# Kernel tuning notes

Hardware: AMD Instinct MI355X
Metric: run time of the kernel (lower is better)

Reference implementation:

```python
import jax, jax.numpy as jnp
import numpy as np

VOCAB, EMBED, HIDDEN, OUT = 50257, 256, 256, 2
BATCH, SEQ = 128, 512


def setup_inputs() -> dict:
    key = jax.random.key(0)
    ks = jax.random.split(key, 8)
    tokens = jax.random.randint(ks[0], (BATCH, SEQ), 0, VOCAB)
    emb = jax.random.normal(ks[1], (VOCAB, EMBED), jnp.float32) * 0.02
    emb = emb.at[VOCAB - 1].set(0.0)  # padding_idx=-1 -> last row zeroed
    s_x = 1.0 / np.sqrt(EMBED)
    s_h = 1.0 / np.sqrt(HIDDEN)
    # gates stacked in order (f, i, c, o): W_x=[W_f;W_i;W_c;W_o], same for U/biases
    W_x = jax.random.uniform(ks[2], (4 * HIDDEN, EMBED), jnp.float32, -s_x, s_x)
    U_h = jax.random.uniform(ks[3], (4 * HIDDEN, HIDDEN), jnp.float32, -s_h, s_h)
    b_x = jax.random.uniform(ks[4], (4 * HIDDEN,), jnp.float32, -s_x, s_x)
    b_u = jax.random.uniform(ks[5], (4 * HIDDEN,), jnp.float32, -s_h, s_h)
    b_g = jnp.zeros((4 * HIDDEN,), jnp.float32)  # extra b_f/b_i/b_c/b_o params
    fc_w = jax.random.uniform(ks[6], (OUT, HIDDEN), jnp.float32, -s_h, s_h)
    fc_b = jax.random.uniform(ks[7], (OUT,), jnp.float32, -s_h, s_h)
    return {"tokens": tokens, "emb": emb, "W_x": W_x, "b_x": b_x,
            "U_h": U_h, "b_u": b_u, "b_g": b_g, "fc_w": fc_w, "fc_b": fc_b}


def reference(tokens, emb, W_x, b_x, U_h, b_u, b_g, fc_w, fc_b):
    H = U_h.shape[1]
    x = emb[tokens]                                   # [B,S,E]
    # precompute all input projections + all constant biases in one GEMM
    xp = jnp.einsum('bse,ge->bsg', x, W_x) + (b_x + b_u + b_g)  # [B,S,4H]
    xp = jnp.swapaxes(xp, 0, 1)                       # [S,B,4H]
    B = tokens.shape[0]
    h0 = jnp.zeros((B, H), x.dtype)
    c0 = jnp.zeros((B, H), x.dtype)

    def step(carry, xp_t):
        h, c = carry
        g = xp_t + h @ U_h.T                          # [B,4H]
        f = jax.nn.sigmoid(g[:, 0 * H:1 * H])
        i = jax.nn.sigmoid(g[:, 1 * H:2 * H])
        c_hat = jnp.tanh(g[:, 2 * H:3 * H])
        o = jax.nn.sigmoid(g[:, 3 * H:4 * H])
        c = f * c + i * c_hat
        h = o * jnp.tanh(c)
        return (h, c), None

    (h_t, _), _ = jax.lax.scan(step, (h0, c0), xp)
    return h_t @ fc_w.T + fc_b                        # [B,OUT]
```

## Files before the change

kernel.cpp:

```cpp
#include <hip/hip_runtime.h>

typedef short short8 __attribute__((ext_vector_type(8)));
typedef float f4 __attribute__((ext_vector_type(4)));

#define BATCH 128
#define SEQ   512
#define EMB   256
#define HID   256
#define G4    1024

static __device__ __forceinline__ unsigned short f2b(float f) {
    union { float f; unsigned int u; } v; v.f = f;
    unsigned int u = v.u;
    return (unsigned short)((u + 0x7FFFu + ((u >> 16) & 1u)) >> 16);
}
static __device__ __forceinline__ float b2f(unsigned short s) {
    union { unsigned int u; float f; } v; v.u = ((unsigned int)s) << 16;
    return v.f;
}

__global__ void prep_kernel(const float* __restrict__ W_x, const float* __restrict__ U_h,
                            const float* __restrict__ b_x, const float* __restrict__ b_u,
                            const float* __restrict__ b_g,
                            unsigned short* __restrict__ w_xb, unsigned short* __restrict__ u_hb,
                            float* __restrict__ bias,
                            unsigned int* __restrict__ hx32, float* __restrict__ out) {
    int i = blockIdx.x * blockDim.x + threadIdx.x;
    if (i < G4 * EMB) w_xb[i] = f2b(W_x[i]);
    if (i < G4 * HID) u_hb[i] = f2b(U_h[i]);
    if (i < G4) bias[i] = b_x[i] + b_u[i] + b_g[i];
    if (i < 65536) hx32[i] = 0;
    if (i < 256) out[i] = 0.0f;
}

__global__ __launch_bounds__(256) void xp_gemm(
    const int* __restrict__ tokens, const float* __restrict__ emb,
    const unsigned short* __restrict__ w_xb, const float* __restrict__ bias,
    unsigned short* __restrict__ xp)
{
    __shared__ unsigned short As[64][264];
    __shared__ unsigned short Bs[64][264];
    __shared__ unsigned short Xs[64][72];
    const int m0 = blockIdx.x * 64;
    const int b  = m0 >> 9;
    const int s0 = m0 & 511;
    const int tid = threadIdx.x;
    const int cS = tid >> 2, qS = (tid & 3) * 64;
    {
        const int tok = tokens[m0 + cS];
        const float* src = emb + (long)tok * EMB + qS;
        #pragma unroll
        for (int i = 0; i < 8; ++i) {
            float4 v0 = ((const float4*)src)[2 * i];
            float4 v1 = ((const float4*)src)[2 * i + 1];
            short8 pk;
            pk[0] = (short)f2b(v0.x); pk[1] = (short)f2b(v0.y);
            pk[2] = (short)f2b(v0.z); pk[3] = (short)f2b(v0.w);
            pk[4] = (short)f2b(v1.x); pk[5] = (short)f2b(v1.y);
            pk[6] = (short)f2b(v1.z); pk[7] = (short)f2b(v1.w);
            *(short8*)&As[cS][qS + i * 8] = pk;
        }
    }
    __syncthreads();
    const int w = tid >> 6, l = tid & 63;
    const int ln = l & 15, hi = l >> 4;
    short8 a[8];
    #pragma unroll
    for (int kk = 0; kk < 8; ++kk)
        a[kk] = *(const short8*)&As[16 * w + ln][kk * 32 + hi * 8];

    const int rl = tid >> 2;
    const int cl = (tid & 3) * 16;

    for (int n0 = 0; n0 < G4; n0 += 64) {
        {
            const unsigned short* src = &w_xb[(size_t)(n0 + cS) * EMB + qS];
            #pragma unroll
            for (int i = 0; i < 8; ++i)
                *(short8*)&Bs[cS][qS + i * 8] = *(const short8*)&src[i * 8];
        }
        __syncthreads();
        f4 acc[4] = {};
        #pragma unroll
        for (int kk = 0; kk < 8; ++kk) {
            #pragma unroll
            for (int nn = 0; nn < 4; ++nn) {
                short8 bfr = *(const short8*)&Bs[nn * 16 + ln][kk * 32 + hi * 8];
                acc[nn] = __builtin_amdgcn_mfma_f32_16x16x32_bf16(a[kk], bfr, acc[nn], 0, 0, 0);
            }
        }
        #pragma unroll
        for (int nn = 0; nn < 4; ++nn) {
            const float bs = bias[n0 + nn * 16 + ln];
            #pragma unroll
            for (int r = 0; r < 4; ++r)
                Xs[16 * w + 4 * hi + r][nn * 16 + ln] = f2b(acc[nn][r] + bs);
        }
        size_t off = ((size_t)(s0 + rl) * BATCH + b) * G4 + n0 + cl;
        *(short8*)&xp[off]     = *(const short8*)&Xs[rl][cl];
        *(short8*)&xp[off + 8] = *(const short8*)&Xs[rl][cl + 8];
        __syncthreads();
    }
}

__global__ void __launch_bounds__(512, 2)
lstm_recur(const unsigned short* __restrict__ xp,
           const unsigned short* __restrict__ u_hb,
           const float* __restrict__ fc_w, const float* __restrict__ fc_b,
           unsigned int* __restrict__ hxw, float* __restrict__ out)
{
    __shared__ unsigned short hsl0[4096];
    __shared__ unsigned short hsl1[4096];
    __shared__ unsigned short xl0[16 * 136];
    __shared__ unsigned short xl1[16 * 136];
    const int tid = threadIdx.x;
    const int w = tid >> 6, l = tid & 63;
    const int ln = l & 15, hi = l >> 4;
    const int bid = blockIdx.x;
    const int g = bid & 7, E = bid >> 3;
    const int lu = w * 4 + hi;

    short8 Br[8];
    int fo[8];
    {
        const int col = (ln & 3) * 256 + E * 32 + w * 4 + (ln >> 2);
        const unsigned short* ubase = u_hb + (size_t)col * HID + hi * 8;
        #pragma unroll
        for (int j = 0; j < 8; ++j) {
            const int s = (E + j) & 7;
            fo[j] = s * 512;
            Br[j] = *(const short8*)&ubase[s * 32];
        }
    }

    for (int i = tid; i < 2048; i += 512) { ((unsigned*)hsl0)[i] = 0; ((unsigned*)hsl1)[i] = 0; }

    const int xrow = tid >> 5, seg4 = tid & 31;
    const size_t xoff = (size_t)(16 * g + xrow) * 1024 + (seg4 >> 3) * 256 + E * 32 + (seg4 & 7) * 4;
    const int xdst = xrow * 136 + (seg4 >> 3) * 32 + (seg4 & 7) * 4;
    *(unsigned long long*)&xl0[xdst] = *(const unsigned long long*)(xp + xoff);
    __syncthreads();

    int pbase[2], pub[2];
    #pragma unroll
    for (int par = 0; par < 2; ++par) {
        pbase[par] = ((par * 8 + g) * 8) * 512 + tid;
        pub[par]   = ((par * 8 + g) * 8 + E) * 512 + lu * 16 + ln;
    }
    int ppq[7];
    #pragma unroll
    for (int d = 0; d < 7; ++d) ppq[d] = (((E + 1 + d) & 7) << 9);
    const int lup = tid >> 4, bp = tid & 15;
    const int sbase = ((lup >> 3) * 16 + bp) * 8 + (lup & 7);
    const int ho = E * 512 + ((lu >> 3) * 16 + ln) * 8 + (lu & 7);
    const int xb = ln * 136 + lu;
    const int fro = l * 8;

    float c0 = 0.0f;

    for (int t = 0; t < SEQ; ++t) {
        const int cur = t & 1;
        unsigned short* hslc = cur ? hsl1 : hsl0;
        unsigned short* hsln = cur ? hsl0 : hsl1;
        const unsigned short* xlc = cur ? xl1 : xl0;
        unsigned short* xln = cur ? xl0 : xl1;

        unsigned int pw[7];
        const unsigned int* ps = hxw;
        if (t > 0) {
            ps = hxw + pbase[cur ^ 1];
            #pragma unroll
            for (int d = 0; d < 7; ++d)
                pw[d] = __hip_atomic_load(ps + ppq[d], __ATOMIC_RELAXED, __HIP_MEMORY_SCOPE_AGENT);
        }
        unsigned long long sv;
        const bool do_stage = (t + 1 < SEQ);
        if (do_stage) sv = *(const unsigned long long*)(xp + (size_t)(t + 1) * 131072 + xoff);

        f4 acc = {};
        {
            short8 hf = *(const short8*)&hslc[fo[0] + fro];
            acc = __builtin_amdgcn_mfma_f32_16x16x32_bf16(Br[0], hf, acc, 0, 0, 0);
        }

        if (t > 0) {
            const unsigned int tag = (unsigned int)t;
            for (;;) {
                unsigned int bad = 0;
                #pragma unroll
                for (int d = 0; d < 7; ++d) bad |= (pw[d] ^ tag);
                if ((bad & 0xffffu) == 0u) break;
                #pragma unroll
                for (int d = 0; d < 7; ++d)
                    pw[d] = __hip_atomic_load(ps + ppq[d], __ATOMIC_RELAXED, __HIP_MEMORY_SCOPE_AGENT);
            }
            #pragma unroll
            for (int d = 0; d < 7; ++d)
                hslc[ppq[d] + sbase] = (unsigned short)(pw[d] >> 16);
        }
        __syncthreads();

        #pragma unroll
        for (int j = 1; j < 8; ++j) {
            short8 hf = *(const short8*)&hslc[fo[j] + fro];
            acc = __builtin_amdgcn_mfma_f32_16x16x32_bf16(Br[j], hf, acc, 0, 0, 0);
        }

        float vf = acc[0] + b2f(xlc[xb]);
        float vi = acc[1] + b2f(xlc[xb + 32]);
        float vc = acc[2] + b2f(xlc[xb + 64]);
        float vo = acc[3] + b2f(xlc[xb + 96]);
        float ea = __expf(-vf), ei = __expf(-vi);
        float eb = __expf(-2.0f * vc), eo = __expf(-vo);
        float rf = __builtin_amdgcn_rcpf(1.0f + ea);
        float it = (1.0f - eb) * __builtin_amdgcn_rcpf((1.0f + ei) * (1.0f + eb));
        float cn = fmaf(rf, c0, it);
        c0 = cn;
        float ed = __expf(-2.0f * cn);
        float h = (1.0f - ed) * __builtin_amdgcn_rcpf((1.0f + eo) * (1.0f + ed));
        unsigned short hb16 = f2b(h);
        hsln[ho] = hb16;
        __hip_atomic_store(hxw + pub[cur], ((unsigned int)hb16 << 16) | (unsigned int)(t + 1),
                           __ATOMIC_RELAXED, __HIP_MEMORY_SCOPE_AGENT);

        if (do_stage) *(unsigned long long*)&xln[xdst] = sv;
        __syncthreads();
    }

    if (tid < 32) {
        const int r = tid >> 1, o = tid & 1;
        float acc_fc = (E == 0) ? fc_b[o] : 0.0f;
        for (int jj = 0; jj < 32; ++jj) {
            float h = b2f(hsl0[E * 512 + ((jj >> 3) * 16 + r) * 8 + (jj & 7)]);
            acc_fc += h * fc_w[o * HID + E * 32 + jj];
        }
        atomicAdd(&out[(16 * g + r) * 2 + o], acc_fc);
    }
}

extern "C" void kernel_launch(void* const* d_in, const int* in_sizes, int n_in,
                              void* d_out, int out_size, void* d_ws, size_t ws_size,
                              hipStream_t stream) {
    const int*   tokens = (const int*)  d_in[0];
    const float* emb    = (const float*)d_in[1];
    const float* W_x    = (const float*)d_in[2];
    const float* b_x    = (const float*)d_in[3];
    const float* U_h    = (const float*)d_in[4];
    const float* b_u    = (const float*)d_in[5];
    const float* b_g    = (const float*)d_in[6];
    const float* fc_w   = (const float*)d_in[7];
    const float* fc_b   = (const float*)d_in[8];
    float* out = (float*)d_out;

    char* ws = (char*)d_ws;
    unsigned short* w_xb  = (unsigned short*)(ws);
    unsigned short* u_hb  = (unsigned short*)(ws + 524288);
    float*          bias  = (float*)(ws + 1048576);
    unsigned int*   hxw   = (unsigned int*)(ws + 1052672);
    unsigned short* xp    = (unsigned short*)(ws + 1314816);

    prep_kernel<<<1024, 256, 0, stream>>>(W_x, U_h, b_x, b_u, b_g, w_xb, u_hb, bias,
                                          hxw, out);
    xp_gemm<<<1024, 256, 0, stream>>>(tokens, emb, w_xb, bias, xp);

    lstm_recur<<<64, 512, 0, stream>>>(xp, u_hb, fc_w, fc_b, hxw, out);
}
```

Before: 663.7 us.

## Split LSTM recurrence across 16 blocks per batch group with smaller blocks

The persistent recurrent kernel now uses 128 blocks of 256 threads: each of 8 batch groups is spread over 16 blocks, each owning 16 hidden units instead of 32. Every block therefore polls and gathers hidden-state slices from 15 peers rather than 7 through tagged atomic words. The split MFMA chain into two independent accumulators shortens the dependent latency. Less work per step per block is traded against more cross-block synchronization traffic and polling per timestep.

```diff
diff --git a/kernel.cpp b/kernel.cpp
--- a/kernel.cpp
+++ b/kernel.cpp
@@ -103,7 +103,7 @@
     }
 }
 
-__global__ void __launch_bounds__(512, 2)
+__global__ void __launch_bounds__(256, 2)
 lstm_recur(const unsigned short* __restrict__ xp,
            const unsigned short* __restrict__ u_hb,
            const float* __restrict__ fc_w, const float* __restrict__ fc_b,
@@ -111,8 +111,8 @@
 {
     __shared__ unsigned short hsl0[4096];
     __shared__ unsigned short hsl1[4096];
-    __shared__ unsigned short xl0[16 * 136];
-    __shared__ unsigned short xl1[16 * 136];
+    __shared__ unsigned short xl0[16 * 68];
+    __shared__ unsigned short xl1[16 * 68];
     const int tid = threadIdx.x;
     const int w = tid >> 6, l = tid & 63;
     const int ln = l & 15, hi = l >> 4;
@@ -121,39 +121,42 @@
     const int lu = w * 4 + hi;
 
     short8 Br[8];
-    int fo[8];
     {
-        const int col = (ln & 3) * 256 + E * 32 + w * 4 + (ln >> 2);
+        const int col = (ln & 3) * 256 + E * 16 + w * 4 + (ln >> 2);
         const unsigned short* ubase = u_hb + (size_t)col * HID + hi * 8;
         #pragma unroll
-        for (int j = 0; j < 8; ++j) {
-            const int s = (E + j) & 7;
-            fo[j] = s * 512;
-            Br[j] = *(const short8*)&ubase[s * 32];
-        }
-    }
-
-    for (int i = tid; i < 2048; i += 512) { ((unsigned*)hsl0)[i] = 0; ((unsigned*)hsl1)[i] = 0; }
-
-    const int xrow = tid >> 5, seg4 = tid & 31;
-    const size_t xoff = (size_t)(16 * g + xrow) * 1024 + (seg4 >> 3) * 256 + E * 32 + (seg4 & 7) * 4;
-    const int xdst = xrow * 136 + (seg4 >> 3) * 32 + (seg4 & 7) * 4;
+        for (int s = 0; s < 8; ++s)
+            Br[s] = *(const short8*)&ubase[s * 32];
+    }
+
+    for (int i = tid; i < 2048; i += 256) { ((unsigned*)hsl0)[i] = 0; ((unsigned*)hsl1)[i] = 0; }
+
+    const int xrow = tid >> 4, seg = tid & 15;
+    const size_t xoff = (size_t)(16 * g + xrow) * 1024 + (seg >> 2) * 256 + E * 16 + (seg & 3) * 4;
+    const int xdst = xrow * 68 + (seg >> 2) * 16 + (seg & 3) * 4;
     *(unsigned long long*)&xl0[xdst] = *(const unsigned long long*)(xp + xoff);
     __syncthreads();
 
     int pbase[2], pub[2];
     #pragma unroll
     for (int par = 0; par < 2; ++par) {
-        pbase[par] = ((par * 8 + g) * 8) * 512 + tid;
-        pub[par]   = ((par * 8 + g) * 8 + E) * 512 + lu * 16 + ln;
-    }
-    int ppq[7];
+        pbase[par] = (par * 8 + g) * 4096 + tid;
+        pub[par]   = (par * 8 + g) * 4096 + E * 256 + lu * 16 + ln;
+    }
+    int ppq[15], sf[15];
+    const int lup = tid >> 4, bp = tid & 15;
     #pragma unroll
-    for (int d = 0; d < 7; ++d) ppq[d] = (((E + 1 + d) & 7) << 9);
-    const int lup = tid >> 4, bp = tid & 15;
-    const int sbase = ((lup >> 3) * 16 + bp) * 8 + (lup & 7);
-    const int ho = E * 512 + ((lu >> 3) * 16 + ln) * 8 + (lu & 7);
-    const int xb = ln * 136 + lu;
+    for (int d = 0; d < 15; ++d) {
+        const int pq = (E + 1 + d) & 15;
+        ppq[d] = pq << 8;
+        const int ug = pq * 16 + lup;
+        const int ss = ug >> 5, k = ug & 31;
+        sf[d] = ss * 512 + ((k >> 3) * 16 + bp) * 8 + (k & 7);
+    }
+    const int ugo = E * 16 + lu;
+    const int ko = ugo & 31;
+    const int ho = (ugo >> 5) * 512 + ((ko >> 3) * 16 + ln) * 8 + (ko & 7);
+    const int xb = ln * 68 + lu;
     const int fro = l * 8;
 
     float c0 = 0.0f;
@@ -165,51 +168,49 @@
         const unsigned short* xlc = cur ? xl1 : xl0;
         unsigned short* xln = cur ? xl0 : xl1;
 
-        unsigned int pw[7];
+        unsigned int pw[15];
         const unsigned int* ps = hxw;
         if (t > 0) {
             ps = hxw + pbase[cur ^ 1];
             #pragma unroll
-            for (int d = 0; d < 7; ++d)
+            for (int d = 0; d < 15; ++d)
                 pw[d] = __hip_atomic_load(ps + ppq[d], __ATOMIC_RELAXED, __HIP_MEMORY_SCOPE_AGENT);
         }
         unsigned long long sv;
         const bool do_stage = (t + 1 < SEQ);
         if (do_stage) sv = *(const unsigned long long*)(xp + (size_t)(t + 1) * 131072 + xoff);
-
-        f4 acc = {};
-        {
-            short8 hf = *(const short8*)&hslc[fo[0] + fro];
-            acc = __builtin_amdgcn_mfma_f32_16x16x32_bf16(Br[0], hf, acc, 0, 0, 0);
-        }
 
         if (t > 0) {
             const unsigned int tag = (unsigned int)t;
             for (;;) {
                 unsigned int bad = 0;
                 #pragma unroll
-                for (int d = 0; d < 7; ++d) bad |= (pw[d] ^ tag);
+                for (int d = 0; d < 15; ++d) bad |= (pw[d] ^ tag);
                 if ((bad & 0xffffu) == 0u) break;
                 #pragma unroll
-                for (int d = 0; d < 7; ++d)
+                for (int d = 0; d < 15; ++d)
                     pw[d] = __hip_atomic_load(ps + ppq[d], __ATOMIC_RELAXED, __HIP_MEMORY_SCOPE_AGENT);
             }
             #pragma unroll
-            for (int d = 0; d < 7; ++d)
-                hslc[ppq[d] + sbase] = (unsigned short)(pw[d] >> 16);
-        }
-        __syncthreads();
-
-        #pragma unroll
-        for (int j = 1; j < 8; ++j) {
-            short8 hf = *(const short8*)&hslc[fo[j] + fro];
-            acc = __builtin_amdgcn_mfma_f32_16x16x32_bf16(Br[j], hf, acc, 0, 0, 0);
-        }
+            for (int d = 0; d < 15; ++d)
+                hslc[sf[d]] = (unsigned short)(pw[d] >> 16);
+        }
+        __syncthreads();
+
+        f4 aa = {}, ab = {};
+        #pragma unroll
+        for (int s = 0; s < 8; s += 2) {
+            short8 h0 = *(const short8*)&hslc[s * 512 + fro];
+            short8 h1 = *(const short8*)&hslc[(s + 1) * 512 + fro];
+            aa = __builtin_amdgcn_mfma_f32_16x16x32_bf16(Br[s], h0, aa, 0, 0, 0);
+            ab = __builtin_amdgcn_mfma_f32_16x16x32_bf16(Br[s + 1], h1, ab, 0, 0, 0);
+        }
+        f4 acc = aa + ab;
 
         float vf = acc[0] + b2f(xlc[xb]);
-        float vi = acc[1] + b2f(xlc[xb + 32]);
-        float vc = acc[2] + b2f(xlc[xb + 64]);
-        float vo = acc[3] + b2f(xlc[xb + 96]);
+        float vi = acc[1] + b2f(xlc[xb + 16]);
+        float vc = acc[2] + b2f(xlc[xb + 32]);
+        float vo = acc[3] + b2f(xlc[xb + 48]);
         float ea = __expf(-vf), ei = __expf(-vi);
         float eb = __expf(-2.0f * vc), eo = __expf(-vo);
         float rf = __builtin_amdgcn_rcpf(1.0f + ea);
@@ -230,9 +231,11 @@
     if (tid < 32) {
         const int r = tid >> 1, o = tid & 1;
         float acc_fc = (E == 0) ? fc_b[o] : 0.0f;
-        for (int jj = 0; jj < 32; ++jj) {
-            float h = b2f(hsl0[E * 512 + ((jj >> 3) * 16 + r) * 8 + (jj & 7)]);
-            acc_fc += h * fc_w[o * HID + E * 32 + jj];
+        for (int jj = 0; jj < 16; ++jj) {
+            const int ug = E * 16 + jj;
+            const int k = ug & 31;
+            float h = b2f(hsl0[(ug >> 5) * 512 + ((k >> 3) * 16 + r) * 8 + (k & 7)]);
+            acc_fc += h * fc_w[o * HID + ug];
         }
         atomicAdd(&out[(16 * g + r) * 2 + o], acc_fc);
     }
@@ -263,5 +266,5 @@
                                           hxw, out);
     xp_gemm<<<1024, 256, 0, stream>>>(tokens, emb, w_xb, bias, xp);
 
-    lstm_recur<<<64, 512, 0, stream>>>(xp, u_hb, fc_w, fc_b, hxw, out);
-}
+    lstm_recur<<<128, 256, 0, stream>>>(xp, u_hb, fc_w, fc_b, hxw, out);
+}
```

After: 932.1 us. 1.4x slower.
